# Performance work log

Hardware: AMD Instinct MI355X
Metric: run time of the kernel (lower is better)

## Reference

```python
import jax, jax.numpy as jnp
import numpy as np

B, C, T = 32, 512, 2048
OUT_SEQ_LEN = 80
SIGMA2 = 10.0


def setup_inputs() -> dict:
    key = jax.random.key(0)
    k1, k2, k3, k4, k5, k6 = jax.random.split(key, 6)
    x = jax.random.normal(k1, (B, C, T), dtype=jnp.float32)
    # lengths in [T//2, T], with at least one equal to T (torch broadcast assumes max(len)==T)
    len_fea = jax.random.randint(k2, (B,), T // 2, T + 1)
    len_fea = len_fea.at[0].set(T)
    s1 = 1.0 / np.sqrt(C)
    conv1_w = jax.random.uniform(k3, (C, C), jnp.float32, -s1, s1)   # 1x1 conv == linear [out,in]
    conv1_b = jax.random.uniform(k4, (C,), jnp.float32, -s1, s1)
    conv2_w = jax.random.uniform(k5, (C,), jnp.float32, -s1, s1)     # out_channels=1, squeezed
    conv2_b = jax.random.uniform(k6, (), jnp.float32, -s1, s1)
    return {"x": x, "len_fea": len_fea, "conv1_w": conv1_w, "conv1_b": conv1_b,
            "conv2_w": conv2_w, "conv2_b": conv2_b}


def reference(x, len_fea, conv1_w, conv1_b, conv2_w, conv2_b):
    b_size, _, Tt = x.shape
    unaligned = x  # [B,C,T]
    h = jax.nn.relu(x)
    h = jnp.einsum('oc,bct->bot', conv1_w, h) + conv1_b[None, :, None]  # 1x1 conv
    h = jax.nn.relu(h)
    g = jnp.einsum('c,bct->bt', conv2_w, h) + conv2_b                   # 1x1 conv to 1 channel
    g = jax.nn.sigmoid(g)                                               # rec=True path
    gls_ends = jnp.cumsum(g, axis=1)            # [B,T]
    gls_centers = gls_ends - g * 0.5            # [B,T]
    aligned_lengths = gls_ends[jnp.arange(b_size), len_fea - 1]         # [B]
    out_pos = 0.5 + jnp.arange(OUT_SEQ_LEN, dtype=x.dtype)              # rec=True positions
    w = gls_centers[:, None, :] - out_pos[None, :, None]                # [B,L,T]
    w = -(w * w) / SIGMA2
    mask = (jnp.arange(Tt)[None, :] >= len_fea[:, None]).astype(x.dtype)  # [B,T]
    w = w - 1e9 * mask[:, None, :]
    w = jax.nn.softmax(w, axis=-1)
    aligned_features = jnp.einsum('blt,bct->blc', w, unaligned)         # [B,L,C]
    return aligned_features, aligned_lengths
```

## Files before the change

kernel.cpp:

```cpp
#include <hip/hip_runtime.h>
#include <hip/hip_bf16.h>

#define NB 32
#define NC 512
#define NT 2048
#define NL 80
static constexpr float kInvSigma2 = 0.1f;

typedef __attribute__((ext_vector_type(8))) __bf16 bf16x8;
typedef __attribute__((ext_vector_type(4))) float f32x4;

__global__ __launch_bounds__(256) void k_w1p(const float* __restrict__ w1,
                                             __hip_bfloat16* __restrict__ w1p) {
  const int q = blockIdx.x * 256 + threadIdx.x;
  const int c_lo = (q & 3) << 3;
  const int o_lo = (q >> 2) & 15;
  const int c5 = (q >> 6) & 15;
  const int o4 = q >> 10;
  const int o = (o4 << 4) + o_lo;
  const int c = (c5 << 5) + c_lo;
  const float4 p0 = *reinterpret_cast<const float4*>(&w1[o * NC + c]);
  const float4 p1 = *reinterpret_cast<const float4*>(&w1[o * NC + c + 4]);
  bf16x8 v;
  v[0] = (__bf16)p0.x; v[1] = (__bf16)p0.y;
  v[2] = (__bf16)p0.z; v[3] = (__bf16)p0.w;
  v[4] = (__bf16)p1.x; v[5] = (__bf16)p1.y;
  v[6] = (__bf16)p1.z; v[7] = (__bf16)p1.w;
  *reinterpret_cast<bf16x8*>(&w1p[(size_t)q * 8]) = v;
}

__global__ __launch_bounds__(512, 4) void k_g_mfma(
    const float* __restrict__ x, const __hip_bfloat16* __restrict__ w1p,
    const float* __restrict__ b1, const float* __restrict__ w2,
    const float* __restrict__ b2, float* __restrict__ g) {
  __shared__ __hip_bfloat16 bs[64 * 512];
  __shared__ float pws[8][64];
  const int blk = blockIdx.x;
  const int b = blk >> 5;
  const int t0 = (blk & 31) << 6;
  const int tid = threadIdx.x;
  const int w = tid >> 6;
  const int lane = tid & 63;
  const int ln = tid & 15;
  const int kg = lane >> 4;
  const int ob = w << 6;

  {
    const int tl = (tid & 15) << 2;
    const int cp = (tid >> 4) << 1;
    const float* xb = x + (size_t)b * NC * NT + t0;
#pragma unroll
    for (int i = 0; i < 8; ++i) {
      const int c = (i << 6) + cp;
      const float4 va =
          *reinterpret_cast<const float4*>(&xb[(size_t)c * NT + tl]);
      const float4 vb =
          *reinterpret_cast<const float4*>(&xb[(size_t)(c + 1) * NT + tl]);
      const float fa[4] = {va.x, va.y, va.z, va.w};
      const float fb[4] = {vb.x, vb.y, vb.z, vb.w};
#pragma unroll
      for (int j = 0; j < 4; ++j) {
        const int t = tl + j;
        const __hip_bfloat16 lo = __float2bfloat16(fmaxf(fa[j], 0.f));
        const __hip_bfloat16 hi = __float2bfloat16(fmaxf(fb[j], 0.f));
        const unsigned pk =
            ((unsigned)*reinterpret_cast<const unsigned short*>(&hi) << 16) |
            *reinterpret_cast<const unsigned short*>(&lo);
        const int gran = ((c >> 3) ^ (t & 7) ^ ((t >> 3) & 7)) & 7;
        const int base = (c >> 3) & ~7;
        *reinterpret_cast<unsigned*>(
            (char*)bs + (t << 10) +
            (((base | gran) << 4) | ((c & 7) << 1))) = pk;
      }
    }
  }
  __syncthreads();

  f32x4 acc[4][4];
#pragma unroll
  for (int ot = 0; ot < 4; ++ot)
#pragma unroll
    for (int nt = 0; nt < 4; ++nt) acc[ot][nt] = (f32x4){0.f, 0.f, 0.f, 0.f};

  int rowb[4], xm[4];
#pragma unroll
  for (int nt = 0; nt < 4; ++nt) {
    const int tr = (nt << 4) + ln;
    rowb[nt] = tr << 10;
    xm[nt] = (((tr & 7) ^ ((tr >> 3) & 7)) & 7) << 4;
  }
  const __hip_bfloat16* abase =
      w1p + ((size_t)w << 15) + (ln << 5) + (kg << 3);
  const char* bsb = (const char*)bs;

#pragma unroll 4
  for (int ks = 0; ks < 16; ++ks) {
    const int gb = (ks << 6) + (kg << 4);
    bf16x8 bfrag[4];
#pragma unroll
    for (int nt = 0; nt < 4; ++nt)
      bfrag[nt] = *reinterpret_cast<const bf16x8*>(
          bsb + rowb[nt] + (gb ^ xm[nt]));
    __builtin_amdgcn_s_setprio(1);
#pragma unroll
    for (int ot = 0; ot < 4; ++ot) {
      const bf16x8 af = *reinterpret_cast<const bf16x8*>(
          abase + (ot << 13) + (ks << 9));
#pragma unroll
      for (int nt = 0; nt < 4; ++nt)
        acc[ot][nt] = __builtin_amdgcn_mfma_f32_16x16x32_bf16(
            af, bfrag[nt], acc[ot][nt], 0, 0, 0);
    }
    __builtin_amdgcn_s_setprio(0);
  }

  float pl[4] = {0.f, 0.f, 0.f, 0.f};
#pragma unroll
  for (int ot = 0; ot < 4; ++ot) {
    const int o4 = ob + (ot << 4) + (kg << 2);
    const float4 b1v = *reinterpret_cast<const float4*>(&b1[o4]);
    const float4 w2v = *reinterpret_cast<const float4*>(&w2[o4]);
#pragma unroll
    for (int nt = 0; nt < 4; ++nt) {
      pl[nt] = fmaf(w2v.x, fmaxf(acc[ot][nt][0] + b1v.x, 0.f), pl[nt]);
      pl[nt] = fmaf(w2v.y, fmaxf(acc[ot][nt][1] + b1v.y, 0.f), pl[nt]);
      pl[nt] = fmaf(w2v.z, fmaxf(acc[ot][nt][2] + b1v.z, 0.f), pl[nt]);
      pl[nt] = fmaf(w2v.w, fmaxf(acc[ot][nt][3] + b1v.w, 0.f), pl[nt]);
    }
  }
#pragma unroll
  for (int nt = 0; nt < 4; ++nt) {
    pl[nt] += __shfl_xor(pl[nt], 16, 64);
    pl[nt] += __shfl_xor(pl[nt], 32, 64);
  }
  if (kg == 0) {
#pragma unroll
    for (int nt = 0; nt < 4; ++nt) pws[w][(nt << 4) + ln] = pl[nt];
  }
  __syncthreads();
  if (tid < 64) {
    float s = b2[0];
#pragma unroll
    for (int i = 0; i < 8; ++i) s += pws[i][tid];
    g[b * NT + t0 + tid] = 1.f / (1.f + __expf(-s));
  }
}

__global__ __launch_bounds__(256) void k_g_slow(const float* __restrict__ x,
                                                const float* __restrict__ w1,
                                                const float* __restrict__ b1,
                                                const float* __restrict__ w2,
                                                const float* __restrict__ b2,
                                                float* __restrict__ g) {
  __shared__ __hip_bfloat16 xs[NC][64];
  const int blk = blockIdx.x;
  const int b = blk >> 5;
  const int t0 = (blk & 31) << 6;
  const int tid = threadIdx.x;
  {
    const int tl = (tid & 15) << 2;
    const int c0 = tid >> 4;
    for (int c = c0; c < NC; c += 16) {
      const float4 v = *reinterpret_cast<const float4*>(
          &x[((size_t)b * NC + c) * NT + t0 + tl]);
      xs[c][tl + 0] = __float2bfloat16(fmaxf(v.x, 0.f));
      xs[c][tl + 1] = __float2bfloat16(fmaxf(v.y, 0.f));
      xs[c][tl + 2] = __float2bfloat16(fmaxf(v.z, 0.f));
      xs[c][tl + 3] = __float2bfloat16(fmaxf(v.w, 0.f));
    }
  }
  __syncthreads();
  const int og = tid >> 6;
  const int t = tid & 63;
  float gacc = 0.f;
  for (int pass = 0; pass < 16; ++pass) {
    const int o0 = (og << 7) + (pass << 3);
    float h[8];
#pragma unroll
    for (int j = 0; j < 8; ++j) h[j] = b1[o0 + j];
    const float* wrow = w1 + (size_t)o0 * NC;
#pragma unroll 4
    for (int c = 0; c < NC; ++c) {
      const float xv = __bfloat162float(xs[c][t]);
#pragma unroll
      for (int j = 0; j < 8; ++j) h[j] = fmaf(wrow[j * NC + c], xv, h[j]);
    }
    float p = 0.f;
#pragma unroll
    for (int j = 0; j < 8; ++j) p = fmaf(w2[o0 + j], fmaxf(h[j], 0.f), p);
    gacc += p;
  }
  __syncthreads();
  float* gr = reinterpret_cast<float*>(&xs[0][0]);
  gr[og * 64 + t] = gacc;
  __syncthreads();
  if (tid < 64) {
    const float s = gr[tid] + gr[64 + tid] + gr[128 + tid] + gr[192 + tid] + b2[0];
    g[b * NT + t0 + tid] = 1.f / (1.f + __expf(-s));
  }
}

__global__ __launch_bounds__(256) void k_scan(const float* __restrict__ g,
                                              const int* __restrict__ len_fea,
                                              float* __restrict__ centers,
                                              float* __restrict__ out_len) {
  const int b = blockIdx.x;
  const int tid = threadIdx.x;
  const float* gb = g + b * NT;
  float v[8];
  {
    const float4 p0 = *reinterpret_cast<const float4*>(&gb[tid * 8]);
    const float4 p1 = *reinterpret_cast<const float4*>(&gb[tid * 8 + 4]);
    v[0] = p0.x; v[1] = p0.y; v[2] = p0.z; v[3] = p0.w;
    v[4] = p1.x; v[5] = p1.y; v[6] = p1.z; v[7] = p1.w;
  }
  float s = 0.f;
#pragma unroll
  for (int j = 0; j < 8; ++j) s += v[j];
  float wscan = s;
  const int lane = tid & 63, wid = tid >> 6;
#pragma unroll
  for (int off = 1; off < 64; off <<= 1) {
    const float o = __shfl_up(wscan, (unsigned)off, 64);
    if (lane >= off) wscan += o;
  }
  __shared__ float wsum[4];
  if (lane == 63) wsum[wid] = wscan;
  __syncthreads();
  float base = 0.f;
#pragma unroll
  for (int i = 0; i < 4; ++i)
    if (i < wid) base += wsum[i];
  float run = base + wscan - s;
  const int li = len_fea[b] - 1;
#pragma unroll
  for (int j = 0; j < 8; ++j) {
    const int t = tid * 8 + j;
    run += v[j];
    centers[b * NT + t] = run - 0.5f * v[j];
    if (t == li) out_len[b] = run;
  }
}

__global__ __launch_bounds__(256) void k_wstats(
    const float* __restrict__ centers, const int* __restrict__ len_fea,
    __hip_bfloat16* __restrict__ wbf) {
  const int b = blockIdx.x / NL;
  const int l = blockIdx.x % NL;
  const int tid = threadIdx.x;
  const int len = len_fea[b];
  const float pos = 0.5f + (float)l;
  const float* cb = centers + b * NT;
  const int t0 = tid * 8;

  float cv[8];
  {
    const float4 p0 = *reinterpret_cast<const float4*>(&cb[t0]);
    const float4 p1 = *reinterpret_cast<const float4*>(&cb[t0 + 4]);
    cv[0] = p0.x; cv[1] = p0.y; cv[2] = p0.z; cv[3] = p0.w;
    cv[4] = p1.x; cv[5] = p1.y; cv[6] = p1.z; cv[7] = p1.w;
  }
  float lg[8];
  float m = -3.0e38f;
#pragma unroll
  for (int j = 0; j < 8; ++j) {
    if (t0 + j < len) {
      const float d = cv[j] - pos;
      lg[j] = -d * d * kInvSigma2;
      m = fmaxf(m, lg[j]);
    } else {
      lg[j] = -3.0e38f;
    }
  }
  const int lane = tid & 63, wid = tid >> 6;
#pragma unroll
  for (int off = 32; off > 0; off >>= 1) m = fmaxf(m, __shfl_xor(m, off, 64));
  __shared__ float redm[4];
  if (lane == 0) redm[wid] = m;
  __syncthreads();
  const float M = fmaxf(fmaxf(redm[0], redm[1]), fmaxf(redm[2], redm[3]));

  float e[8];
  float ssum = 0.f;
#pragma unroll
  for (int j = 0; j < 8; ++j) {
    e[j] = (t0 + j < len) ? __expf(lg[j] - M) : 0.f;
    ssum += e[j];
  }
#pragma unroll
  for (int off = 32; off > 0; off >>= 1) ssum += __shfl_xor(ssum, off, 64);
  __shared__ float reds[4];
  if (lane == 0) reds[wid] = ssum;
  __syncthreads();
  const float rinv = 1.f / (reds[0] + reds[1] + reds[2] + reds[3]);

  bf16x8 o;
#pragma unroll
  for (int j = 0; j < 8; ++j) o[j] = (__bf16)(e[j] * rinv);
  *reinterpret_cast<bf16x8*>(&wbf[((size_t)b * NL + l) * NT + t0]) = o;
}

__global__ __launch_bounds__(256) void k_out_mfma(
    const float* __restrict__ x, const __hip_bfloat16* __restrict__ wbf,
    float* __restrict__ out) {
  __shared__ float red[3][64][41];
  const int blk = blockIdx.x;
  const int b = blk >> 4;
  const int c0 = (blk & 15) << 5;
  const int tid = threadIdx.x;
  const int w = tid >> 6;
  const int lane = tid & 63;
  const int ln = tid & 15;
  const int kg = lane >> 4;
  const int tbase = w << 9;

  f32x4 acc[5][2];
#pragma unroll
  for (int lt = 0; lt < 5; ++lt)
#pragma unroll
    for (int nt = 0; nt < 2; ++nt) acc[lt][nt] = (f32x4){0.f, 0.f, 0.f, 0.f};

  const __hip_bfloat16* abase =
      wbf + ((size_t)b * NL + ln) * NT + tbase + (kg << 3);
  const float* bbase = x + ((size_t)b * NC + c0 + ln) * NT + tbase + (kg << 3);

#pragma unroll 4
  for (int ks = 0; ks < 16; ++ks) {
    const int ck = ks << 5;
    bf16x8 bfrag[2];
#pragma unroll
    for (int nt = 0; nt < 2; ++nt) {
      const float4 p0 =
          *reinterpret_cast<const float4*>(bbase + nt * 16 * NT + ck);
      const float4 p1 =
          *reinterpret_cast<const float4*>(bbase + nt * 16 * NT + ck + 4);
      bf16x8 v;
      v[0] = (__bf16)p0.x; v[1] = (__bf16)p0.y;
      v[2] = (__bf16)p0.z; v[3] = (__bf16)p0.w;
      v[4] = (__bf16)p1.x; v[5] = (__bf16)p1.y;
      v[6] = (__bf16)p1.z; v[7] = (__bf16)p1.w;
      bfrag[nt] = v;
    }
#pragma unroll
    for (int lt = 0; lt < 5; ++lt) {
      const bf16x8 af =
          *reinterpret_cast<const bf16x8*>(abase + lt * 16 * NT + ck);
      acc[lt][0] = __builtin_amdgcn_mfma_f32_16x16x32_bf16(af, bfrag[0],
                                                           acc[lt][0], 0, 0, 0);
      acc[lt][1] = __builtin_amdgcn_mfma_f32_16x16x32_bf16(af, bfrag[1],
                                                           acc[lt][1], 0, 0, 0);
    }
  }

  if (w > 0) {
#pragma unroll
    for (int lt = 0; lt < 5; ++lt)
#pragma unroll
      for (int nt = 0; nt < 2; ++nt)
#pragma unroll
        for (int j = 0; j < 4; ++j)
          red[w - 1][lane][lt * 8 + nt * 4 + j] = acc[lt][nt][j];
  }
  __syncthreads();
  if (w == 0) {
#pragma unroll
    for (int lt = 0; lt < 5; ++lt)
#pragma unroll
      for (int nt = 0; nt < 2; ++nt)
#pragma unroll
        for (int j = 0; j < 4; ++j) {
          float s = acc[lt][nt][j];
#pragma unroll
          for (int i = 0; i < 3; ++i) s += red[i][lane][lt * 8 + nt * 4 + j];
          const int l = lt * 16 + (kg << 2) + j;
          out[((size_t)b * NL + l) * NC + c0 + nt * 16 + ln] = s;
        }
  }
}

__global__ __launch_bounds__(256) void k_stats(const float* __restrict__ centers,
                                               const int* __restrict__ len_fea,
                                               float* __restrict__ rmax,
                                               float* __restrict__ rinv) {
  const int b = blockIdx.x / NL;
  const int l = blockIdx.x % NL;
  const int tid = threadIdx.x;
  const int len = len_fea[b];
  const float pos = 0.5f + (float)l;
  const float* cb = centers + b * NT;
  float lg[8];
  float m = -3.0e38f;
  const int t0 = tid * 8;
#pragma unroll
  for (int j = 0; j < 8; ++j) {
    const int t = t0 + j;
    if (t < len) {
      const float d = cb[t] - pos;
      lg[j] = -d * d * kInvSigma2;
      m = fmaxf(m, lg[j]);
    } else {
      lg[j] = -3.0e38f;
    }
  }
  const int lane = tid & 63, wid = tid >> 6;
#pragma unroll
  for (int off = 32; off > 0; off >>= 1) m = fmaxf(m, __shfl_xor(m, off, 64));
  __shared__ float redm[4];
  if (lane == 0) redm[wid] = m;
  __syncthreads();
  const float M = fmaxf(fmaxf(redm[0], redm[1]), fmaxf(redm[2], redm[3]));
  float ssum = 0.f;
#pragma unroll
  for (int j = 0; j < 8; ++j) {
    if (t0 + j < len) ssum += __expf(lg[j] - M);
  }
#pragma unroll
  for (int off = 32; off > 0; off >>= 1) ssum += __shfl_xor(ssum, off, 64);
  __shared__ float reds[4];
  if (lane == 0) reds[wid] = ssum;
  __syncthreads();
  if (tid == 0) {
    const float S = reds[0] + reds[1] + reds[2] + reds[3];
    rmax[blockIdx.x] = M;
    rinv[blockIdx.x] = 1.f / S;
  }
}

__global__ __launch_bounds__(128) void k_out(const float* __restrict__ x,
                                             const int* __restrict__ len_fea,
                                             const float* __restrict__ centers,
                                             const float* __restrict__ rmax,
                                             const float* __restrict__ rinv,
                                             float* __restrict__ out) {
  __shared__ float xsh[128][65];
  __shared__ float wsh[20][64];
  const int blk = blockIdx.x;
  const int b = blk >> 4;
  const int l0 = ((blk >> 2) & 3) * 20;
  const int c0 = (blk & 3) * 128;
  const int tid = threadIdx.x;
  const int len = len_fea[b];
  float acc[20];
#pragma unroll
  for (int l = 0; l < 20; ++l) acc[l] = 0.f;

  for (int t0 = 0; t0 < NT; t0 += 64) {
    __syncthreads();
    {
      const int tl = (tid & 15) << 2;
      const int r0 = tid >> 4;
      for (int r = r0; r < 128; r += 8) {
        const float4 v = *reinterpret_cast<const float4*>(
            &x[((size_t)b * NC + c0 + r) * NT + t0 + tl]);
        float* p = &xsh[r][tl];
        p[0] = v.x; p[1] = v.y; p[2] = v.z; p[3] = v.w;
      }
    }
#pragma unroll
    for (int k = 0; k < 10; ++k) {
      const int idx = k * 128 + tid;
      const int l = idx >> 6;
      const int tt = idx & 63;
      float wv = 0.f;
      if (t0 + tt < len) {
        const float d = centers[b * NT + t0 + tt] - (0.5f + (float)(l0 + l));
        wv = __expf(-d * d * kInvSigma2 - rmax[b * NL + l0 + l]) *
             rinv[b * NL + l0 + l];
      }
      wsh[l][tt] = wv;
    }
    __syncthreads();
#pragma unroll 4
    for (int tt = 0; tt < 64; ++tt) {
      const float xv = xsh[tid][tt];
#pragma unroll
      for (int l = 0; l < 20; ++l) acc[l] = fmaf(wsh[l][tt], xv, acc[l]);
    }
  }
#pragma unroll
  for (int l = 0; l < 20; ++l)
    out[((size_t)b * NL + l0 + l) * NC + c0 + tid] = acc[l];
}

extern "C" void kernel_launch(void* const* d_in, const int* in_sizes, int n_in,
                              void* d_out, int out_size, void* d_ws, size_t ws_size,
                              hipStream_t stream) {
  const float* x = (const float*)d_in[0];
  const int* len_fea = (const int*)d_in[1];
  const float* w1 = (const float*)d_in[2];
  const float* b1 = (const float*)d_in[3];
  const float* w2 = (const float*)d_in[4];
  const float* b2 = (const float*)d_in[5];

  float* out = (float*)d_out;
  float* out_len = out + (size_t)NB * NL * NC;

  float* ws = (float*)d_ws;
  float* g = ws;
  float* centers = ws + NB * NT;
  float* rmax = ws + 2 * NB * NT;
  float* rinv = rmax + NB * NL;
  __hip_bfloat16* w1p = (__hip_bfloat16*)(rinv + NB * NL);
  __hip_bfloat16* wbf = w1p + (size_t)NC * NC;

  const size_t need_mid = (size_t)(2 * NB * NT + 2 * NB * NL) * 4 +
                          (size_t)NC * NC * 2;
  const size_t need_full = need_mid + (size_t)NB * NL * NT * 2;

  if (ws_size >= need_full) {
    k_w1p<<<(NC * NC) / 2048, 256, 0, stream>>>(w1, w1p);
    k_g_mfma<<<NB * 32, 512, 0, stream>>>(x, w1p, b1, w2, b2, g);
    k_scan<<<NB, 256, 0, stream>>>(g, len_fea, centers, out_len);
    k_wstats<<<NB * NL, 256, 0, stream>>>(centers, len_fea, wbf);
    k_out_mfma<<<NB * 16, 256, 0, stream>>>(x, wbf, out);
  } else if (ws_size >= need_mid) {
    k_w1p<<<(NC * NC) / 2048, 256, 0, stream>>>(w1, w1p);
    k_g_mfma<<<NB * 32, 512, 0, stream>>>(x, w1p, b1, w2, b2, g);
    k_scan<<<NB, 256, 0, stream>>>(g, len_fea, centers, out_len);
    k_stats<<<NB * NL, 256, 0, stream>>>(centers, len_fea, rmax, rinv);
    k_out<<<NB * 16, 128, 0, stream>>>(x, len_fea, centers, rmax, rinv, out);
  } else {
    k_g_slow<<<NB * 32, 256, 0, stream>>>(x, w1, b1, w2, b2, g);
    k_scan<<<NB, 256, 0, stream>>>(g, len_fea, centers, out_len);
    k_stats<<<NB * NL, 256, 0, stream>>>(centers, len_fea, rmax, rinv);
    k_out<<<NB * 16, 128, 0, stream>>>(x, len_fea, centers, rmax, rinv, out);
  }
}
```

Baseline: 105.0 us.

## Make gate GEMM kernel persistent over four tiles with double-buffered LDS prefetch

The gate kernel now launches 256 blocks, each processing four consecutive 64-timestep tiles, instead of one block per tile. The next tile's x values are loaded into registers during the current tile's MFMA loop and written into a second LDS buffer, so global loads overlap compute. The cost is twice the LDS per block and more registers, with launch bounds lowered from 4 to 2 blocks per SM. Fewer blocks may also leave some CUs idle on a large GPU.

```diff
diff --git a/kernel.cpp b/kernel.cpp
--- a/kernel.cpp
+++ b/kernel.cpp
@@ -29,15 +29,12 @@
   *reinterpret_cast<bf16x8*>(&w1p[(size_t)q * 8]) = v;
 }
 
-__global__ __launch_bounds__(512, 4) void k_g_mfma(
+__global__ __launch_bounds__(512, 2) void k_g_mfma(
     const float* __restrict__ x, const __hip_bfloat16* __restrict__ w1p,
     const float* __restrict__ b1, const float* __restrict__ w2,
     const float* __restrict__ b2, float* __restrict__ g) {
-  __shared__ __hip_bfloat16 bs[64 * 512];
+  __shared__ __hip_bfloat16 bs[2][64 * 512];
   __shared__ float pws[8][64];
-  const int blk = blockIdx.x;
-  const int b = blk >> 5;
-  const int t0 = (blk & 31) << 6;
   const int tid = threadIdx.x;
   const int w = tid >> 6;
   const int lane = tid & 63;
@@ -45,19 +42,31 @@
   const int kg = lane >> 4;
   const int ob = w << 6;
 
-  {
-    const int tl = (tid & 15) << 2;
-    const int cp = (tid >> 4) << 1;
-    const float* xb = x + (size_t)b * NC * NT + t0;
+  const int tl = (tid & 15) << 2;
+  const int cp = (tid >> 4) << 1;
+
+  const int tile0 = blockIdx.x << 2;
+
+  float4 va[8], vb[8];
+
+  auto issue = [&](int tile) {
+    const float* xb =
+        x + (size_t)(tile >> 5) * NC * NT + ((tile & 31) << 6);
 #pragma unroll
     for (int i = 0; i < 8; ++i) {
       const int c = (i << 6) + cp;
-      const float4 va =
-          *reinterpret_cast<const float4*>(&xb[(size_t)c * NT + tl]);
-      const float4 vb =
-          *reinterpret_cast<const float4*>(&xb[(size_t)(c + 1) * NT + tl]);
-      const float fa[4] = {va.x, va.y, va.z, va.w};
-      const float fb[4] = {vb.x, vb.y, vb.z, vb.w};
+      va[i] = *reinterpret_cast<const float4*>(&xb[(size_t)c * NT + tl]);
+      vb[i] = *reinterpret_cast<const float4*>(&xb[(size_t)(c + 1) * NT + tl]);
+    }
+  };
+
+  auto writeLDS = [&](int buf) {
+    char* base = (char*)&bs[buf][0];
+#pragma unroll
+    for (int i = 0; i < 8; ++i) {
+      const int c = (i << 6) + cp;
+      const float fa[4] = {va[i].x, va[i].y, va[i].z, va[i].w};
+      const float fb[4] = {vb[i].x, vb[i].y, vb[i].z, vb[i].w};
 #pragma unroll
       for (int j = 0; j < 4; ++j) {
         const int t = tl + j;
@@ -67,20 +76,12 @@
             ((unsigned)*reinterpret_cast<const unsigned short*>(&hi) << 16) |
             *reinterpret_cast<const unsigned short*>(&lo);
         const int gran = ((c >> 3) ^ (t & 7) ^ ((t >> 3) & 7)) & 7;
-        const int base = (c >> 3) & ~7;
+        const int bse = (c >> 3) & ~7;
         *reinterpret_cast<unsigned*>(
-            (char*)bs + (t << 10) +
-            (((base | gran) << 4) | ((c & 7) << 1))) = pk;
+            base + (t << 10) + (((bse | gran) << 4) | ((c & 7) << 1))) = pk;
       }
     }
-  }
-  __syncthreads();
-
-  f32x4 acc[4][4];
-#pragma unroll
-  for (int ot = 0; ot < 4; ++ot)
-#pragma unroll
-    for (int nt = 0; nt < 4; ++nt) acc[ot][nt] = (f32x4){0.f, 0.f, 0.f, 0.f};
+  };
 
   int rowb[4], xm[4];
 #pragma unroll
@@ -91,58 +92,78 @@
   }
   const __hip_bfloat16* abase =
       w1p + ((size_t)w << 15) + (ln << 5) + (kg << 3);
-  const char* bsb = (const char*)bs;
-
+
+  issue(tile0);
+  writeLDS(0);
+  __syncthreads();
+
+  for (int i = 0; i < 4; ++i) {
+    const int tile = tile0 + i;
+    if (i < 3) issue(tile + 1);
+    __builtin_amdgcn_sched_barrier(0);
+
+    f32x4 acc[4][4];
+#pragma unroll
+    for (int ot = 0; ot < 4; ++ot)
+#pragma unroll
+      for (int nt = 0; nt < 4; ++nt) acc[ot][nt] = (f32x4){0.f, 0.f, 0.f, 0.f};
+
+    const char* bsb = (const char*)&bs[i & 1][0];
 #pragma unroll 4
-  for (int ks = 0; ks < 16; ++ks) {
-    const int gb = (ks << 6) + (kg << 4);
-    bf16x8 bfrag[4];
-#pragma unroll
-    for (int nt = 0; nt < 4; ++nt)
-      bfrag[nt] = *reinterpret_cast<const bf16x8*>(
-          bsb + rowb[nt] + (gb ^ xm[nt]));
-    __builtin_amdgcn_s_setprio(1);
+    for (int ks = 0; ks < 16; ++ks) {
+      const int gb = (ks << 6) + (kg << 4);
+      bf16x8 bfrag[4];
+#pragma unroll
+      for (int nt = 0; nt < 4; ++nt)
+        bfrag[nt] = *reinterpret_cast<const bf16x8*>(
+            bsb + rowb[nt] + (gb ^ xm[nt]));
+      __builtin_amdgcn_s_setprio(1);
+#pragma unroll
+      for (int ot = 0; ot < 4; ++ot) {
+        const bf16x8 af = *reinterpret_cast<const bf16x8*>(
+            abase + (ot << 13) + (ks << 9));
+#pragma unroll
+        for (int nt = 0; nt < 4; ++nt)
+          acc[ot][nt] = __builtin_amdgcn_mfma_f32_16x16x32_bf16(
+              af, bfrag[nt], acc[ot][nt], 0, 0, 0);
+      }
+      __builtin_amdgcn_s_setprio(0);
+    }
+
+    float pl[4] = {0.f, 0.f, 0.f, 0.f};
 #pragma unroll
     for (int ot = 0; ot < 4; ++ot) {
-      const bf16x8 af = *reinterpret_cast<const bf16x8*>(
-          abase + (ot << 13) + (ks << 9));
-#pragma unroll
-      for (int nt = 0; nt < 4; ++nt)
-        acc[ot][nt] = __builtin_amdgcn_mfma_f32_16x16x32_bf16(
-            af, bfrag[nt], acc[ot][nt], 0, 0, 0);
-    }
-    __builtin_amdgcn_s_setprio(0);
-  }
-
-  float pl[4] = {0.f, 0.f, 0.f, 0.f};
-#pragma unroll
-  for (int ot = 0; ot < 4; ++ot) {
-    const int o4 = ob + (ot << 4) + (kg << 2);
-    const float4 b1v = *reinterpret_cast<const float4*>(&b1[o4]);
-    const float4 w2v = *reinterpret_cast<const float4*>(&w2[o4]);
+      const int o4 = ob + (ot << 4) + (kg << 2);
+      const float4 b1v = *reinterpret_cast<const float4*>(&b1[o4]);
+      const float4 w2v = *reinterpret_cast<const float4*>(&w2[o4]);
+#pragma unroll
+      for (int nt = 0; nt < 4; ++nt) {
+        pl[nt] = fmaf(w2v.x, fmaxf(acc[ot][nt][0] + b1v.x, 0.f), pl[nt]);
+        pl[nt] = fmaf(w2v.y, fmaxf(acc[ot][nt][1] + b1v.y, 0.f), pl[nt]);
+        pl[nt] = fmaf(w2v.z, fmaxf(acc[ot][nt][2] + b1v.z, 0.f), pl[nt]);
+        pl[nt] = fmaf(w2v.w, fmaxf(acc[ot][nt][3] + b1v.w, 0.f), pl[nt]);
+      }
+    }
 #pragma unroll
     for (int nt = 0; nt < 4; ++nt) {
-      pl[nt] = fmaf(w2v.x, fmaxf(acc[ot][nt][0] + b1v.x, 0.f), pl[nt]);
-      pl[nt] = fmaf(w2v.y, fmaxf(acc[ot][nt][1] + b1v.y, 0.f), pl[nt]);
-      pl[nt] = fmaf(w2v.z, fmaxf(acc[ot][nt][2] + b1v.z, 0.f), pl[nt]);
-      pl[nt] = fmaf(w2v.w, fmaxf(acc[ot][nt][3] + b1v.w, 0.f), pl[nt]);
-    }
-  }
-#pragma unroll
-  for (int nt = 0; nt < 4; ++nt) {
-    pl[nt] += __shfl_xor(pl[nt], 16, 64);
-    pl[nt] += __shfl_xor(pl[nt], 32, 64);
-  }
-  if (kg == 0) {
-#pragma unroll
-    for (int nt = 0; nt < 4; ++nt) pws[w][(nt << 4) + ln] = pl[nt];
-  }
-  __syncthreads();
-  if (tid < 64) {
-    float s = b2[0];
-#pragma unroll
-    for (int i = 0; i < 8; ++i) s += pws[i][tid];
-    g[b * NT + t0 + tid] = 1.f / (1.f + __expf(-s));
+      pl[nt] += __shfl_xor(pl[nt], 16, 64);
+      pl[nt] += __shfl_xor(pl[nt], 32, 64);
+    }
+    if (kg == 0) {
+#pragma unroll
+      for (int nt = 0; nt < 4; ++nt) pws[w][(nt << 4) + ln] = pl[nt];
+    }
+    __syncthreads();
+
+    if (i < 3) writeLDS((i + 1) & 1);
+    if (tid < 64) {
+      float s = b2[0];
+#pragma unroll
+      for (int q = 0; q < 8; ++q) s += pws[q][tid];
+      g[(tile >> 5) * NT + ((tile & 31) << 6) + tid] =
+          1.f / (1.f + __expf(-s));
+    }
+    __syncthreads();
   }
 }
 
@@ -509,13 +530,13 @@
 
   if (ws_size >= need_full) {
     k_w1p<<<(NC * NC) / 2048, 256, 0, stream>>>(w1, w1p);
-    k_g_mfma<<<NB * 32, 512, 0, stream>>>(x, w1p, b1, w2, b2, g);
+    k_g_mfma<<<256, 512, 0, stream>>>(x, w1p, b1, w2, b2, g);
     k_scan<<<NB, 256, 0, stream>>>(g, len_fea, centers, out_len);
     k_wstats<<<NB * NL, 256, 0, stream>>>(centers, len_fea, wbf);
     k_out_mfma<<<NB * 16, 256, 0, stream>>>(x, wbf, out);
   } else if (ws_size >= need_mid) {
     k_w1p<<<(NC * NC) / 2048, 256, 0, stream>>>(w1, w1p);
-    k_g_mfma<<<NB * 32, 512, 0, stream>>>(x, w1p, b1, w2, b2, g);
+    k_g_mfma<<<256, 512, 0, stream>>>(x, w1p, b1, w2, b2, g);
     k_scan<<<NB, 256, 0, stream>>>(g, len_fea, centers, out_len);
     k_stats<<<NB * NL, 256, 0, stream>>>(centers, len_fea, rmax, rinv);
     k_out<<<NB * 16, 128, 0, stream>>>(x, len_fea, centers, rmax, rinv, out);
```

Measured after the change: 149.3 us. 1.42x slower.
